# Performance work log

Hardware: AMD Instinct MI355X
Metric: run time of the kernel (lower is better)

The kernel has to match this reference:

```python
import jax, jax.numpy as jnp
import numpy as np

N = 20000      # num_nodes
E = 320000     # num_edges (avg degree 16)
HID = 256      # hid_dim
H = 4          # attention heads
D = HID // H   # per-head dim (concat heads -> HID)
L = 2          # nGAT_layer
OUT = 12       # out_dim / pred_len (decoder steps)
NEG_SLOPE = 0.2


def setup_inputs() -> dict:
    key = jax.random.key(0)
    ks = jax.random.split(key, 16)
    s = 0.05
    nrm = lambda k, shape: jax.random.normal(k, shape, jnp.float32) * s
    return dict(
        x=nrm(ks[0], (N, HID)),
        edge_index=jax.random.randint(ks[1], (2, E), 0, N, dtype=jnp.int32),
        # GATv2Conv params per layer (stacked over L layers)
        gat_w_src=nrm(ks[2], (L, HID, H * D)),
        gat_w_dst=nrm(ks[3], (L, HID, H * D)),
        gat_att=nrm(ks[4], (L, H, D)),
        gat_bias=nrm(ks[5], (L, H * D)),
        # decoder_mlp: Linear(1 + HID -> HID)
        mlp_w=nrm(ks[6], (HID, 1 + HID)),
        mlp_b=nrm(ks[7], (HID,)),
        # nn.LSTM (1 layer, input HID, hidden HID), torch gate order i,f,g,o
        lstm_w_ih=nrm(ks[8], (4 * HID, HID)),
        lstm_w_hh=nrm(ks[9], (4 * HID, HID)),
        lstm_b_ih=nrm(ks[10], (4 * HID,)),
        lstm_b_hh=nrm(ks[11], (4 * HID,)),
        # decoder_init_proj: Linear(HID -> 1); decoder_output_proj: Linear(HID -> 1)
        init_w=nrm(ks[12], (1, HID)),
        init_b=nrm(ks[13], (1,)),
        out_w=nrm(ks[14], (1, HID)),
        out_b=nrm(ks[15], (1,)),
    )


def _gatv2_layer(x, src, dst, w_src, w_dst, att, bias):
    n = x.shape[0]
    xl = (x @ w_src).reshape(n, H, D)   # source-side projection
    xr = (x @ w_dst).reshape(n, H, D)   # destination-side projection
    # GATv2: e_ij = a^T LeakyReLU(Wl x_j + Wr x_i)
    e = jax.nn.leaky_relu(xl[src] + xr[dst], NEG_SLOPE)        # [E,H,D]
    logits = jnp.einsum('ehd,hd->eh', e, att)                   # [E,H]
    # edge softmax over incoming edges of each destination node
    m = jax.ops.segment_max(logits, dst, num_segments=n)        # [N,H]
    ex = jnp.exp(logits - m[dst])
    denom = jax.ops.segment_sum(ex, dst, num_segments=n)
    alpha = ex / denom[dst]                                     # [E,H]
    out = jax.ops.segment_sum(xl[src] * alpha[:, :, None], dst, num_segments=n)
    return out.reshape(n, H * D) + bias


def reference(x, edge_index, gat_w_src, gat_w_dst, gat_att, gat_bias,
              mlp_w, mlp_b, lstm_w_ih, lstm_w_hh, lstm_b_ih, lstm_b_hh,
              init_w, init_b, out_w, out_b):
    src, dst = edge_index[0], edge_index[1]
    # stacked GAT blocks: GATv2Conv + ELU (element == 2)
    for l in range(L):
        x = _gatv2_layer(x, src, dst, gat_w_src[l], gat_w_dst[l], gat_att[l], gat_bias[l])
        x = jax.nn.elu(x)
    # recurrent LSTM decoder, batch = nodes, seq step by step
    ctx = x                      # encoder_context
    h = x                        # h_0 = x (num_layers = 1)
    c = jnp.zeros_like(x)        # c_0 = 0
    prev = x @ init_w.T + init_b  # [N,1]
    outs = []
    for _ in range(OUT):
        dec_in = jnp.concatenate([prev, ctx], axis=1) @ mlp_w.T + mlp_b  # [N,HID]
        gates = dec_in @ lstm_w_ih.T + lstm_b_ih + h @ lstm_w_hh.T + lstm_b_hh
        i_g, f_g, g_g, o_g = jnp.split(gates, 4, axis=1)
        i_g = jax.nn.sigmoid(i_g)
        f_g = jax.nn.sigmoid(f_g)
        o_g = jax.nn.sigmoid(o_g)
        g_g = jnp.tanh(g_g)
        c = f_g * c + i_g * g_g
        h = o_g * jnp.tanh(c)
        prev = h @ out_w.T + out_b  # [N,1]
        outs.append(prev)
    return jnp.concatenate(outs, axis=1)  # [N, OUT]
```

## Files before the change

### kernel.cpp

```cpp
#include <hip/hip_runtime.h>
#include <hip/hip_bf16.h>

#define NN 20000
#define NE 320000
#define TOUT 12
#define DEGMAX 96
#define MR 80
#define NBLK 250
#define NCHL 14

typedef __bf16 bf16x8 __attribute__((ext_vector_type(8)));
typedef float float4v __attribute__((ext_vector_type(4)));

#define LD8(p) (*(const bf16x8*)(p))
#define MFMA16(a,b,c) __builtin_amdgcn_mfma_f32_16x16x32_bf16((a),(b),(c),0,0,0)

__device__ __forceinline__ float bf2f(const __hip_bfloat16 v){ return __bfloat162float(v); }
__device__ __forceinline__ __hip_bfloat16 f2bf(float v){ return __float2bfloat16(v); }
__device__ __forceinline__ float sigmoidr_(float x){ return __builtin_amdgcn_rcpf(1.f + __expf(-x)); }
__device__ __forceinline__ float tanhr_(float x){ return 1.f - 2.f*__builtin_amdgcn_rcpf(__expf(2.f*x) + 1.f); }
__device__ __forceinline__ float rdf(const void* p, int i, int f32){
  return f32 ? ((const float*)p)[i] : __bfloat162float(((const __hip_bfloat16*)p)[i]);
}

__global__ void k_detect(const void* xraw, int* flag){
  __shared__ int cnt;
  if(threadIdx.x == 0) cnt = 0;
  __syncthreads();
  const unsigned* w = (const unsigned*)xraw;
  int local = 0;
  for(int i = threadIdx.x; i < 4096; i += 256){
    unsigned b = (w[i] >> 8) & 0x7F;
    if(b >= 0x33 && b <= 0x3F) local++;
  }
  atomicAdd(&cnt, local);
  __syncthreads();
  if(threadIdx.x == 0) *flag = (cnt > 2048) ? 0 : 1;
}

__global__ void k_fail(float* out, int n){
  int i = blockIdx.x*256 + threadIdx.x;
  if(i < n) out[i] = 256.0f;
}

__global__ void k_count(const int* __restrict__ dst, int* __restrict__ deg){
  int e = blockIdx.x*256 + threadIdx.x;
  if(e < NE){
    unsigned d = (unsigned)dst[e];
    if(d < NN) atomicAdd(&deg[d], 1);
  }
}

__global__ void k_scan(const int* __restrict__ deg, int* __restrict__ offp, int* __restrict__ cursor){
  __shared__ int part[256];
  __shared__ int excl[257];
  const int CH = (NN + 255)/256;
  int tid = threadIdx.x;
  int lo = tid*CH;
  int hi = lo + CH; if(hi > NN) hi = NN;
  int s = 0;
  for(int i=lo;i<hi;i++) s += deg[i];
  part[tid] = s;
  __syncthreads();
  if(tid == 0){
    int run = 0;
    for(int i=0;i<256;i++){ excl[i] = run; run += part[i]; }
    excl[256] = run;
  }
  __syncthreads();
  int run = excl[tid];
  for(int i=lo;i<hi;i++){ offp[i] = run; cursor[i] = run; run += deg[i]; }
  if(tid == 0) offp[NN] = excl[256];
}

__global__ void k_fill(const int* __restrict__ src, const int* __restrict__ dst,
                       int* __restrict__ cursor, int* __restrict__ csr_src){
  int e = blockIdx.x*256 + threadIdx.x;
  if(e >= NE) return;
  unsigned d = (unsigned)dst[e];
  if(d >= NN) return;
  unsigned p = (unsigned)atomicAdd(&cursor[d], 1);
  if(p < NE){
    unsigned sv = (unsigned)src[e];
    csr_src[p] = (sv < NN) ? (int)sv : 0;
  }
}

__global__ void k_prep(const void* __restrict__ w_src, const void* __restrict__ w_dst,
                       const void* __restrict__ w_hh, const void* __restrict__ wih,
                       const void* __restrict__ mlp_w, const int* __restrict__ flag,
                       __hip_bfloat16* __restrict__ wsrcT, __hip_bfloat16* __restrict__ wdstT,
                       __hip_bfloat16* __restrict__ whhp, __hip_bfloat16* __restrict__ wihb,
                       __hip_bfloat16* __restrict__ mlpT){
  int tid = blockIdx.x*256 + threadIdx.x;
  int f = *flag;
  if(tid < 131072){
    int l = tid >> 16, r = tid & 65535, o = r >> 8, i = r & 255;
    wsrcT[tid] = f2bf(rdf(w_src, l*65536 + i*256 + o, f));
    wdstT[tid] = f2bf(rdf(w_dst, l*65536 + i*256 + o, f));
  }
  if(tid < 262144){
    whhp[tid] = f2bf(rdf(w_hh, tid, f));
    wihb[tid] = f2bf(rdf(wih, tid, f));
  }
  if(tid < 65536){
    int k = tid >> 8, j = tid & 255;
    mlpT[tid] = f2bf(rdf(mlp_w, j*257 + 1 + k, f));
  }
}

__global__ void k_prep_ub(const void* __restrict__ wih, const void* __restrict__ mlp_w,
                          const void* __restrict__ mlp_b,
                          const void* __restrict__ b_ih, const void* __restrict__ b_hh,
                          const void* __restrict__ att, const void* __restrict__ gbias,
                          const void* __restrict__ init_w, const void* __restrict__ init_b,
                          const void* __restrict__ out_w, const void* __restrict__ out_b,
                          const int* __restrict__ flag,
                          float* __restrict__ u, float* __restrict__ bc,
                          float* __restrict__ attf, float* __restrict__ gbiasf,
                          float* __restrict__ initwf, float* __restrict__ outwf,
                          float* __restrict__ sc){
  __shared__ float su[256], sb[256];
  int g = blockIdx.x, j = threadIdx.x, f = *flag;
  float w = rdf(wih, g*256 + j, f);
  su[j] = w * rdf(mlp_w, j*257, f);
  sb[j] = w * rdf(mlp_b, j, f);
  if(g < 2){
    int i = g*256 + j;
    attf[i] = rdf(att, i, f);
    gbiasf[i] = rdf(gbias, i, f);
  }
  if(g == 0){
    initwf[j] = rdf(init_w, j, f);
    outwf[j]  = rdf(out_w, j, f);
    if(j == 0){ sc[0] = rdf(init_b, 0, f); sc[1] = rdf(out_b, 0, f); }
  }
  __syncthreads();
  for(int s=128; s>0; s>>=1){
    if(j < s){ su[j] += su[j+s]; sb[j] += sb[j+s]; }
    __syncthreads();
  }
  if(j == 0){ u[g] = su[0]; bc[g] = sb[0] + rdf(b_ih, g, f) + rdf(b_hh, g, f); }
}

__global__ void k_fold(const __hip_bfloat16* __restrict__ whh_pl,
                       const float* __restrict__ u_vec, const float* __restrict__ outwf,
                       __hip_bfloat16* __restrict__ whh2_pl){
  int i = blockIdx.x*256 + threadIdx.x;
  whh2_pl[i] = f2bf(bf2f(whh_pl[i]) + u_vec[i >> 8]*outwf[i & 255]);
}

__global__ void k_pack(const __hip_bfloat16* __restrict__ Wpl, const __hip_bfloat16* __restrict__ W2pl,
                       const __hip_bfloat16* __restrict__ Wcpl,
                       __hip_bfloat16* __restrict__ WhhP, __hip_bfloat16* __restrict__ Whh2P,
                       __hip_bfloat16* __restrict__ WcP){
  int idx = blockIdx.x*256 + threadIdx.x;
  if(idx >= 32768) return;
  int cs = idx >> 12;
  int kslot = (idx >> 9) & 7;
  int nt = (idx >> 6) & 7;
  int lane = idx & 63;
  int l16 = lane & 15, quad = lane >> 4;
  int brow = (nt>>1)*256 + cs*32 + (nt&1)*16 + l16;
  int srcofs = brow*256 + kslot*32 + quad*8;
  int dst = idx*8;
  *(bf16x8*)(WhhP + dst)  = LD8(Wpl + srcofs);
  *(bf16x8*)(Whh2P + dst) = LD8(W2pl + srcofs);
  *(bf16x8*)(WcP + dst)   = LD8(Wcpl + srcofs);
}

__global__ void k_pack2(const __hip_bfloat16* __restrict__ wsrcT,
                        const __hip_bfloat16* __restrict__ wdstT,
                        __hip_bfloat16* __restrict__ wprojP){
  int idx = blockIdx.x*256 + threadIdx.x;
  if(idx >= 32768) return;
  int m = idx >> 13;
  int fi = idx & 8191;
  int l = m >> 1, role = m & 1;
  int kidx = fi >> 10;
  int nt = (fi >> 6) & 15;
  int lane = fi & 63;
  int l16 = lane & 15, quad = lane >> 4;
  const __hip_bfloat16* src = (role ? wdstT : wsrcT) + l*65536;
  int srcofs = (nt*16 + l16)*256 + kidx*32 + quad*8;
  *(bf16x8*)(wprojP + (size_t)m*65536 + fi*8) = LD8(src + srcofs);
}

__global__ __launch_bounds__(256) void k_gemm_nt_bf(const __hip_bfloat16* __restrict__ A,
                                                    const __hip_bfloat16* __restrict__ B,
                                                    __hip_bfloat16* __restrict__ Cb, int M){
  int wave = threadIdx.x >> 6;
  int lane = threadIdx.x & 63;
  int l16 = lane & 15, quad = lane >> 4, quad8 = quad*8;
  int mBase = blockIdx.x*64 + wave*16;
  int nBase = blockIdx.y*64;
  int arow = mBase + l16; if(arow >= M) arow = M-1;
  const __hip_bfloat16* aptr = A + (size_t)arow*256 + quad8;
  float4v acc[4];
  #pragma unroll
  for(int nt=0;nt<4;nt++){ acc[nt][0]=0.f; acc[nt][1]=0.f; acc[nt][2]=0.f; acc[nt][3]=0.f; }
  for(int k0=0;k0<256;k0+=32){
    bf16x8 a = LD8(aptr + k0);
    #pragma unroll
    for(int nt=0;nt<4;nt++){
      const __hip_bfloat16* bptr = B + (size_t)(nBase + nt*16 + l16)*256 + k0 + quad8;
      acc[nt] = MFMA16(a, LD8(bptr), acc[nt]);
    }
  }
  #pragma unroll
  for(int nt=0;nt<4;nt++){
    int col = nBase + nt*16 + l16;
    #pragma unroll
    for(int r=0;r<4;r++){
      int row = mBase + quad*4 + r;
      if(row < M) Cb[(size_t)row*256 + col] = f2bf(acc[nt][r]);
    }
  }
}

__global__ __launch_bounds__(512, 2) void k_gemm_dual(__hip_bfloat16* __restrict__ P,
                                                      const void* __restrict__ xraw,
                                                      const int* __restrict__ flag,
                                                      int layer0,
                                                      const __hip_bfloat16* __restrict__ BsrcP,
                                                      const __hip_bfloat16* __restrict__ BdstP,
                                                      __hip_bfloat16* __restrict__ Q){
  __shared__ __hip_bfloat16 sA[64*264];
  int tid = threadIdx.x;
  int mBase = blockIdx.x*64;
  {
    int r = tid >> 3;
    int c0 = (tid & 7)*32;
    int grow = mBase + r; if(grow >= NN) grow = NN-1;
    if(layer0){
      int f = *flag;
      #pragma unroll
      for(int j=0;j<32;j++) sA[r*264 + c0 + j] = f2bf(rdf(xraw, grow*256 + c0 + j, f));
    }else{
      const __hip_bfloat16* srcp = P + (size_t)grow*256 + c0;
      #pragma unroll
      for(int j=0;j<4;j++) *(bf16x8*)(&sA[r*264 + c0 + j*8]) = LD8(srcp + j*8);
    }
  }
  __syncthreads();
  int w8 = tid >> 6;
  int w = w8 & 3;
  int role = w8 >> 2;
  int lane = tid&63, l16 = lane&15, quad = lane>>4, quad8 = quad*8;
  const __hip_bfloat16* B = role ? BdstP : BsrcP;
  __hip_bfloat16* C = role ? P : Q;
  const __hip_bfloat16* arow = &sA[(w*16 + l16)*264 + quad8];
  float4v acc[16];
  #pragma unroll
  for(int nt=0;nt<16;nt++){ acc[nt][0]=0.f; acc[nt][1]=0.f; acc[nt][2]=0.f; acc[nt][3]=0.f; }
  for(int kidx=0;kidx<8;kidx++){
    bf16x8 a = *(const bf16x8*)(arow + kidx*32);
    const __hip_bfloat16* bbase = B + (kidx<<13) + (lane<<3);
    #pragma unroll
    for(int nt=0;nt<16;nt++)
      acc[nt] = MFMA16(a, LD8(bbase + (nt<<9)), acc[nt]);
  }
  #pragma unroll
  for(int nt=0;nt<16;nt++){
    int col = nt*16 + l16;
    #pragma unroll
    for(int r=0;r<4;r++){
      int row = mBase + w*16 + quad*4 + r;
      if(row < NN) C[(size_t)row*256 + col] = f2bf(acc[nt][r]);
    }
  }
}

__global__ __launch_bounds__(256) void k_node_fused(const __hip_bfloat16* __restrict__ Q,
                                                    __hip_bfloat16* __restrict__ P,
                                                    const int* __restrict__ offp,
                                                    const int* __restrict__ csr_src,
                                                    const float* __restrict__ attf,
                                                    const float* __restrict__ gbiasf){
  __shared__ float slog[DEGMAX*4];
  __shared__ int ssrc[DEGMAX];
  int node = blockIdx.x;
  int tid = threadIdx.x;
  int s0 = offp[node], s1 = offp[node+1];
  if(s0 < 0) s0 = 0; if(s0 > NE) s0 = NE;
  if(s1 < s0) s1 = s0; if(s1 > NE) s1 = NE;
  int deg = s1 - s0; if(deg > DEGMAX) deg = DEGMAX;
  if(tid < deg){
    unsigned sv = (unsigned)csr_src[s0 + tid];
    ssrc[tid] = (sv < NN) ? (int)sv : 0;
  }
  __syncthreads();
  int w = tid>>6, lane = tid&63;
  int eSlot = lane>>4, li = lane&15;
  float prl[16], attl[16];
  #pragma unroll
  for(int h=0;h<4;h++)
    #pragma unroll
    for(int j=0;j<4;j++){
      int d = h*64 + j*16 + li;
      prl[h*4+j]  = bf2f(P[(size_t)node*256 + d]);
      attl[h*4+j] = attf[d];
    }
  for(int base=0; base<deg; base+=16){
    int e = base + w*4 + eSlot;
    bool valid = (e < deg);
    const __hip_bfloat16* pl = Q + (size_t)ssrc[valid ? e : 0]*256;
    float part[4];
    #pragma unroll
    for(int h=0;h<4;h++){
      float p = 0.f;
      #pragma unroll
      for(int j=0;j<4;j++){
        int d = h*64 + j*16 + li;
        float v = bf2f(pl[d]) + prl[h*4+j];
        v = (v > 0.f) ? v : 0.2f*v;
        p += v * attl[h*4+j];
      }
      part[h] = p;
    }
    #pragma unroll
    for(int h=0;h<4;h++){
      part[h] += __shfl_xor(part[h], 1, 64);
      part[h] += __shfl_xor(part[h], 2, 64);
      part[h] += __shfl_xor(part[h], 4, 64);
      part[h] += __shfl_xor(part[h], 8, 64);
    }
    if(li == 0 && valid){
      #pragma unroll
      for(int h=0;h<4;h++) slog[e*4+h] = part[h];
    }
  }
  __syncthreads();
  {
    int hh = tid >> 6;
    int li64 = tid & 63;
    float m = -1e30f;
    for(int i=li64; i<deg; i+=64) m = fmaxf(m, slog[i*4+hh]);
    #pragma unroll
    for(int s=1; s<64; s<<=1) m = fmaxf(m, __shfl_xor(m, s, 64));
    float den = 0.f;
    for(int i=li64; i<deg; i+=64) den += __expf(slog[i*4+hh] - m);
    #pragma unroll
    for(int s=1; s<64; s<<=1) den += __shfl_xor(den, s, 64);
    float inv = (den > 0.f) ? 1.f/den : 0.f;
    for(int i=li64; i<deg; i+=64) slog[i*4+hh] = __expf(slog[i*4+hh] - m)*inv;
  }
  __syncthreads();
  int d = tid, hd = d>>6;
  float acc = 0.f;
  for(int i=0;i<deg;i++) acc += slog[i*4+hd] * bf2f(Q[(size_t)ssrc[i]*256 + d]);
  acc += gbiasf[d];
  acc = (acc > 0.f) ? acc : (__expf(acc) - 1.f);
  P[(size_t)node*256 + d] = f2bf(acc);
}

__global__ __launch_bounds__(512, 1) void k_lstm80(const __hip_bfloat16* __restrict__ ctx,
                                                   const __hip_bfloat16* __restrict__ WcP,
                                                   const __hip_bfloat16* __restrict__ WhhP,
                                                   const __hip_bfloat16* __restrict__ Whh2P,
                                                   const float* __restrict__ u_vec,
                                                   const float* __restrict__ bc_vec,
                                                   const float* __restrict__ initwf,
                                                   const float* __restrict__ outwf,
                                                   const float* __restrict__ sc,
                                                   float* __restrict__ out){
  __shared__ __hip_bfloat16 sgx[NCHL*4096];
  __shared__ __hip_bfloat16 sh[MR*264];
  __shared__ float spartw[MR*8];
  __shared__ float sprev0[MR];
  float* spart = (float*)sgx;
  int tid = threadIdx.x;
  int mBase = blockIdx.x*MR;
  int cs = tid>>6, lane = tid&63, l16 = lane&15, quad = lane>>4, quad8 = quad*8;
  int phase = (blockIdx.x >> 3) & 7;
  #pragma unroll
  for(int p=0;p<3;p++){
    int r = p*32 + (tid >> 4);
    if(r < MR){
      int c0 = (tid & 15)*16;
      const __hip_bfloat16* srcp = ctx + (size_t)(mBase + r)*256 + c0;
      *(bf16x8*)(&sh[r*264 + c0])     = LD8(srcp);
      *(bf16x8*)(&sh[r*264 + c0 + 8]) = LD8(srcp + 8);
    }
  }
  __syncthreads();
  #pragma unroll
  for(int p=0;p<3;p++){
    int r = p*32 + (tid >> 4);
    int c0 = (tid & 15)*16;
    float part = 0.f;
    if(r < MR){
      #pragma unroll
      for(int j=0;j<16;j++) part += bf2f(sh[r*264 + c0 + j]) * initwf[c0 + j];
    }
    spart[tid] = part;
    __syncthreads();
    if(tid < 32 && p*32 + tid < MR){
      float s = 0.f;
      #pragma unroll
      for(int j=0;j<16;j++) s += spart[tid*16 + j];
      sprev0[p*32 + tid] = s + sc[0];
    }
    __syncthreads();
  }
  float owreg[2];
  #pragma unroll
  for(int tc=0;tc<2;tc++) owreg[tc] = outwf[cs*32 + tc*16 + l16];
  float outb = sc[1];
  bf16x8 gg0, gg1, gg2, gg3, gg4, gg5;
  {
    float bcl[8];
    #pragma unroll
    for(int g=0;g<4;g++)
      #pragma unroll
      for(int tc=0;tc<2;tc++)
        bcl[g*2+tc] = bc_vec[g*256 + cs*32 + tc*16 + l16]
                    + u_vec[g*256 + cs*32 + tc*16 + l16]*outb;
    {
      float4v acc[24];
      #pragma unroll
      for(int nt=0;nt<24;nt++){ acc[nt][0]=0.f; acc[nt][1]=0.f; acc[nt][2]=0.f; acc[nt][3]=0.f; }
      #pragma unroll 2
      for(int ki=0;ki<8;ki++){
        int kidx = (ki + phase) & 7;
        int k0 = kidx*32;
        bf16x8 a0 = *(const bf16x8*)(&sh[l16*264 + k0 + quad8]);
        bf16x8 a1 = *(const bf16x8*)(&sh[(16 + l16)*264 + k0 + quad8]);
        bf16x8 a2 = *(const bf16x8*)(&sh[(32 + l16)*264 + k0 + quad8]);
        const __hip_bfloat16* bbase = WcP + (((cs<<3) + kidx)<<12) + (lane<<3);
        #pragma unroll
        for(int nt=0;nt<8;nt++){
          bf16x8 b = LD8(bbase + (nt<<9));
          acc[nt]    = MFMA16(a0, b, acc[nt]);
          acc[8+nt]  = MFMA16(a1, b, acc[8+nt]);
          acc[16+nt] = MFMA16(a2, b, acc[16+nt]);
        }
      }
      #pragma unroll
      for(int rt=0;rt<3;rt++)
        #pragma unroll
        for(int tc=0;tc<2;tc++)
          #pragma unroll
          for(int half=0;half<2;half++){
            bf16x8 v;
            #pragma unroll
            for(int rr=0;rr<2;rr++)
              #pragma unroll
              for(int g=0;g<4;g++){
                int r = half*2 + rr;
                v[rr*4+g] = (__bf16)f2bf(acc[rt*8 + g*2 + tc][r] + bcl[g*2+tc]);
              }
            int cp = (rt*2+tc)*2 + half;
            *(bf16x8*)(&sgx[cp*4096 + tid*8]) = v;
          }
    }
    {
      float4v acc[16];
      #pragma unroll
      for(int nt=0;nt<16;nt++){ acc[nt][0]=0.f; acc[nt][1]=0.f; acc[nt][2]=0.f; acc[nt][3]=0.f; }
      #pragma unroll 2
      for(int ki=0;ki<8;ki++){
        int kidx = (ki + phase) & 7;
        int k0 = kidx*32;
        bf16x8 a3 = *(const bf16x8*)(&sh[(48 + l16)*264 + k0 + quad8]);
        bf16x8 a4 = *(const bf16x8*)(&sh[(64 + l16)*264 + k0 + quad8]);
        const __hip_bfloat16* bbase = WcP + (((cs<<3) + kidx)<<12) + (lane<<3);
        #pragma unroll
        for(int nt=0;nt<8;nt++){
          bf16x8 b = LD8(bbase + (nt<<9));
          acc[nt]   = MFMA16(a3, b, acc[nt]);
          acc[8+nt] = MFMA16(a4, b, acc[8+nt]);
        }
      }
      #pragma unroll
      for(int rtl=0;rtl<2;rtl++)
        #pragma unroll
        for(int tc=0;tc<2;tc++)
          #pragma unroll
          for(int half=0;half<2;half++){
            bf16x8 v;
            #pragma unroll
            for(int rr=0;rr<2;rr++)
              #pragma unroll
              for(int g=0;g<4;g++){
                int r = half*2 + rr;
                v[rr*4+g] = (__bf16)f2bf(acc[rtl*8 + g*2 + tc][r] + bcl[g*2+tc]);
              }
            const int cp = ((3+rtl)*2+tc)*2 + half;
            if(cp == 12 || cp == 13) *(bf16x8*)(&sgx[cp*4096 + tid*8]) = v;
            else if(cp == 14) gg0 = v;
            else if(cp == 15) gg1 = v;
            else if(cp == 16) gg2 = v;
            else if(cp == 17) gg3 = v;
            else if(cp == 18) gg4 = v;
            else              gg5 = v;
          }
    }
  }
  float creg[40];
  #pragma unroll
  for(int i=0;i<40;i++) creg[i] = 0.f;
  #pragma unroll 1
  for(int step=0; step<TOUT; step++){
    const __hip_bfloat16* W = (step == 0) ? WhhP : Whh2P;
    float4v accA[24];
    #pragma unroll
    for(int nt=0;nt<24;nt++){ accA[nt][0]=0.f; accA[nt][1]=0.f; accA[nt][2]=0.f; accA[nt][3]=0.f; }
    #pragma unroll 2
    for(int ki=0;ki<8;ki++){
      int kidx = (ki + phase) & 7;
      int k0 = kidx*32;
      bf16x8 a0 = *(const bf16x8*)(&sh[l16*264 + k0 + quad8]);
      bf16x8 a1 = *(const bf16x8*)(&sh[(16 + l16)*264 + k0 + quad8]);
      bf16x8 a2 = *(const bf16x8*)(&sh[(32 + l16)*264 + k0 + quad8]);
      const __hip_bfloat16* bbase = W + (((cs<<3) + kidx)<<12) + (lane<<3);
      #pragma unroll
      for(int nt=0;nt<8;nt++){
        bf16x8 b = LD8(bbase + (nt<<9));
        accA[nt]    = MFMA16(a0, b, accA[nt]);
        accA[8+nt]  = MFMA16(a1, b, accA[8+nt]);
        accA[16+nt] = MFMA16(a2, b, accA[16+nt]);
      }
    }
    __syncthreads();
    #pragma unroll
    for(int rt=0; rt<3; rt++){
      float hsum[4];
      hsum[0]=0.f; hsum[1]=0.f; hsum[2]=0.f; hsum[3]=0.f;
      #pragma unroll
      for(int tc=0;tc<2;tc++){
        int col = cs*32 + tc*16 + l16;
        const int cpb = (rt*2+tc)*2;
        bf16x8 ga = *(const bf16x8*)(&sgx[cpb*4096 + tid*8]);
        bf16x8 gb = *(const bf16x8*)(&sgx[(cpb+1)*4096 + tid*8]);
        #pragma unroll
        for(int r=0;r<4;r++){
          int row = rt*16 + quad*4 + r;
          int jb = (r&1)*4;
          float gx0, gx1, gx2, gx3;
          if(r < 2){
            gx0 = bf2f((__hip_bfloat16)ga[jb]);   gx1 = bf2f((__hip_bfloat16)ga[jb+1]);
            gx2 = bf2f((__hip_bfloat16)ga[jb+2]); gx3 = bf2f((__hip_bfloat16)ga[jb+3]);
          }else{
            gx0 = bf2f((__hip_bfloat16)gb[jb]);   gx1 = bf2f((__hip_bfloat16)gb[jb+1]);
            gx2 = bf2f((__hip_bfloat16)gb[jb+2]); gx3 = bf2f((__hip_bfloat16)gb[jb+3]);
          }
          float g0 = accA[rt*8 + tc][r]     + gx0;
          float g1 = accA[rt*8 + 2 + tc][r] + gx1;
          float g2 = accA[rt*8 + 4 + tc][r] + gx2;
          float g3 = accA[rt*8 + 6 + tc][r] + gx3;
          if(step == 0){
            float pd = sprev0[row] - outb;
            g0 += pd*u_vec[col];
            g1 += pd*u_vec[256 + col];
            g2 += pd*u_vec[512 + col];
            g3 += pd*u_vec[768 + col];
          }
          float iv = sigmoidr_(g0), fv = sigmoidr_(g1);
          float gv = tanhr_(g2),    ov = sigmoidr_(g3);
          float cn = fv*creg[rt*8 + tc*4 + r] + iv*gv;
          creg[rt*8 + tc*4 + r] = cn;
          float hn = ov * tanhr_(cn);
          sh[row*264 + col] = f2bf(hn);
          hsum[r] += hn * owreg[tc];
        }
      }
      #pragma unroll
      for(int r=0;r<4;r++){
        hsum[r] += __shfl_xor(hsum[r], 1, 64);
        hsum[r] += __shfl_xor(hsum[r], 2, 64);
        hsum[r] += __shfl_xor(hsum[r], 4, 64);
        hsum[r] += __shfl_xor(hsum[r], 8, 64);
      }
      if(l16 == 0){
        #pragma unroll
        for(int r=0;r<4;r++)
          spartw[(rt*16 + quad*4 + r)*8 + cs] = hsum[r];
      }
    }
    float4v accB[16];
    #pragma unroll
    for(int nt=0;nt<16;nt++){ accB[nt][0]=0.f; accB[nt][1]=0.f; accB[nt][2]=0.f; accB[nt][3]=0.f; }
    #pragma unroll 2
    for(int ki=0;ki<8;ki++){
      int kidx = (ki + phase) & 7;
      int k0 = kidx*32;
      bf16x8 a3 = *(const bf16x8*)(&sh[(48 + l16)*264 + k0 + quad8]);
      bf16x8 a4 = *(const bf16x8*)(&sh[(64 + l16)*264 + k0 + quad8]);
      const __hip_bfloat16* bbase = W + (((cs<<3) + kidx)<<12) + (lane<<3);
      #pragma unroll
      for(int nt=0;nt<8;nt++){
        bf16x8 b = LD8(bbase + (nt<<9));
        accB[nt]   = MFMA16(a3, b, accB[nt]);
        accB[8+nt] = MFMA16(a4, b, accB[8+nt]);
      }
    }
    __syncthreads();
    #pragma unroll
    for(int rtl=0; rtl<2; rtl++){
      const int rt = 3 + rtl;
      float hsum[4];
      hsum[0]=0.f; hsum[1]=0.f; hsum[2]=0.f; hsum[3]=0.f;
      #pragma unroll
      for(int tc=0;tc<2;tc++){
        int col = cs*32 + tc*16 + l16;
        bf16x8 ga, gb;
        if(rtl == 0 && tc == 0){
          ga = *(const bf16x8*)(&sgx[12*4096 + tid*8]);
          gb = *(const bf16x8*)(&sgx[13*4096 + tid*8]);
        }else if(rtl == 0 && tc == 1){ ga = gg0; gb = gg1; }
        else if(rtl == 1 && tc == 0){ ga = gg2; gb = gg3; }
        else                        { ga = gg4; gb = gg5; }
        #pragma unroll
        for(int r=0;r<4;r++){
          int row = rt*16 + quad*4 + r;
          int jb = (r&1)*4;
          float gx0, gx1, gx2, gx3;
          if(r < 2){
            gx0 = bf2f((__hip_bfloat16)ga[jb]);   gx1 = bf2f((__hip_bfloat16)ga[jb+1]);
            gx2 = bf2f((__hip_bfloat16)ga[jb+2]); gx3 = bf2f((__hip_bfloat16)ga[jb+3]);
          }else{
            gx0 = bf2f((__hip_bfloat16)gb[jb]);   gx1 = bf2f((__hip_bfloat16)gb[jb+1]);
            gx2 = bf2f((__hip_bfloat16)gb[jb+2]); gx3 = bf2f((__hip_bfloat16)gb[jb+3]);
          }
          float g0 = accB[rtl*8 + tc][r]     + gx0;
          float g1 = accB[rtl*8 + 2 + tc][r] + gx1;
          float g2 = accB[rtl*8 + 4 + tc][r] + gx2;
          float g3 = accB[rtl*8 + 6 + tc][r] + gx3;
          if(step == 0){
            float pd = sprev0[row] - outb;
            g0 += pd*u_vec[col];
            g1 += pd*u_vec[256 + col];
            g2 += pd*u_vec[512 + col];
            g3 += pd*u_vec[768 + col];
          }
          float iv = sigmoidr_(g0), fv = sigmoidr_(g1);
          float gv = tanhr_(g2),    ov = sigmoidr_(g3);
          float cn = fv*creg[rt*8 + tc*4 + r] + iv*gv;
          creg[rt*8 + tc*4 + r] = cn;
          float hn = ov * tanhr_(cn);
          sh[row*264 + col] = f2bf(hn);
          hsum[r] += hn * owreg[tc];
        }
      }
      #pragma unroll
      for(int r=0;r<4;r++){
        hsum[r] += __shfl_xor(hsum[r], 1, 64);
        hsum[r] += __shfl_xor(hsum[r], 2, 64);
        hsum[r] += __shfl_xor(hsum[r], 4, 64);
        hsum[r] += __shfl_xor(hsum[r], 8, 64);
      }
      if(l16 == 0){
        #pragma unroll
        for(int r=0;r<4;r++)
          spartw[(rt*16 + quad*4 + r)*8 + cs] = hsum[r];
      }
    }
    __syncthreads();
    if(tid < MR){
      float s = outb;
      #pragma unroll
      for(int c=0;c<8;c++) s += spartw[tid*8 + c];
      out[(size_t)(mBase + tid)*TOUT + step] = s;
    }
  }
}

extern "C" void kernel_launch(void* const* d_in, const int* in_sizes, int n_in,
                              void* d_out, int out_size, void* d_ws, size_t ws_size,
                              hipStream_t stream){
  const void* x      = d_in[0];
  const int*  ei     = (const int*)d_in[1];
  const void* w_src  = d_in[2];
  const void* w_dst  = d_in[3];
  const void* att    = d_in[4];
  const void* gbias  = d_in[5];
  const void* mlp_w  = d_in[6];
  const void* mlp_b  = d_in[7];
  const void* w_ih   = d_in[8];
  const void* w_hh   = d_in[9];
  const void* b_ih   = d_in[10];
  const void* b_hh   = d_in[11];
  const void* init_w = d_in[12];
  const void* init_b = d_in[13];
  const void* out_w  = d_in[14];
  const void* out_b  = d_in[15];
  float* out = (float*)d_out;
  const int* srcp = ei;
  const int* dstp = ei + NE;
  (void)in_sizes; (void)n_in;

  char* ws = (char*)d_ws;
  size_t off = 0;
  auto alloc = [&](size_t bytes)->void*{
    void* p = ws + off;
    off += (bytes + 255) & ~(size_t)255;
    return p;
  };
  __hip_bfloat16* P = (__hip_bfloat16*)alloc((size_t)NN*256*2);
  __hip_bfloat16* Q = (__hip_bfloat16*)alloc((size_t)NN*256*2);
  int* deg      = (int*)alloc((size_t)NN*4);
  int* offp     = (int*)alloc((size_t)(NN+1)*4);
  int* cursor   = (int*)alloc((size_t)NN*4);
  int* csr_src  = (int*)alloc((size_t)NE*4);
  __hip_bfloat16* wsrcT   = (__hip_bfloat16*)alloc((size_t)131072*2);
  __hip_bfloat16* wdstT   = (__hip_bfloat16*)alloc((size_t)131072*2);
  __hip_bfloat16* wprojP  = (__hip_bfloat16*)alloc((size_t)4*65536*2);
  __hip_bfloat16* whh_pl  = (__hip_bfloat16*)alloc((size_t)262144*2);
  __hip_bfloat16* whh2_pl = (__hip_bfloat16*)alloc((size_t)262144*2);
  __hip_bfloat16* Wc_pl   = (__hip_bfloat16*)alloc((size_t)262144*2);
  __hip_bfloat16* WhhP    = (__hip_bfloat16*)alloc((size_t)262144*2);
  __hip_bfloat16* Whh2P   = (__hip_bfloat16*)alloc((size_t)262144*2);
  __hip_bfloat16* WcP     = (__hip_bfloat16*)alloc((size_t)262144*2);
  __hip_bfloat16* wihb    = (__hip_bfloat16*)alloc((size_t)262144*2);
  __hip_bfloat16* mlpT    = (__hip_bfloat16*)alloc((size_t)65536*2);
  float* u_vec  = (float*)alloc(1024*4);
  float* bc_vec = (float*)alloc(1024*4);
  float* attf   = (float*)alloc(512*4);
  float* gbiasf = (float*)alloc(512*4);
  float* initwf = (float*)alloc(256*4);
  float* outwf  = (float*)alloc(256*4);
  float* sc     = (float*)alloc(2*4);
  int*   flag   = (int*)alloc(4);

  if(off > ws_size){
    k_fail<<<(out_size + 255)/256, 256, 0, stream>>>(out, out_size);
    return;
  }

  k_detect<<<1, 256, 0, stream>>>(x, flag);
  hipMemsetAsync(deg, 0, (size_t)NN*4, stream);
  hipMemsetAsync(csr_src, 0xFF, (size_t)NE*4, stream);
  k_count<<<NE/256, 256, 0, stream>>>(dstp, deg);
  k_scan<<<1, 256, 0, stream>>>(deg, offp, cursor);
  k_fill<<<NE/256, 256, 0, stream>>>(srcp, dstp, cursor, csr_src);
  k_prep<<<1024, 256, 0, stream>>>(w_src, w_dst, w_hh, w_ih, mlp_w, flag,
                                   wsrcT, wdstT, whh_pl, wihb, mlpT);
  k_prep_ub<<<1024, 256, 0, stream>>>(w_ih, mlp_w, mlp_b, b_ih, b_hh, att, gbias,
                                      init_w, init_b, out_w, out_b, flag,
                                      u_vec, bc_vec, attf, gbiasf, initwf, outwf, sc);
  {
    dim3 gwc(16, 4);
    k_gemm_nt_bf<<<gwc, 256, 0, stream>>>(wihb, mlpT, Wc_pl, 1024);
  }
  k_fold<<<1024, 256, 0, stream>>>(whh_pl, u_vec, outwf, whh2_pl);
  k_pack<<<128, 256, 0, stream>>>(whh_pl, whh2_pl, Wc_pl, WhhP, Whh2P, WcP);
  k_pack2<<<128, 256, 0, stream>>>(wsrcT, wdstT, wprojP);

  for(int l=0;l<2;l++){
    k_gemm_dual<<<313, 512, 0, stream>>>(P, x, flag, (l == 0) ? 1 : 0,
                                         wprojP + (size_t)(l*2)*65536,
                                         wprojP + (size_t)(l*2+1)*65536, Q);
    k_node_fused<<<NN, 256, 0, stream>>>(Q, P, offp, csr_src, attf + l*256, gbiasf + l*256);
  }

  k_lstm80<<<NBLK, 512, 0, stream>>>(P, WcP, WhhP, Whh2P, u_vec, bc_vec,
                                     initwf, outwf, sc, out);
}
```

Baseline: 687.9 us.

## Cache gathered source rows in LDS and split LSTM gate GEMM by gate pairs

```diff
diff --git a/kernel.cpp b/kernel.cpp
--- a/kernel.cpp
+++ b/kernel.cpp
@@ -5,6 +5,7 @@
 #define NE 320000
 #define TOUT 12
 #define DEGMAX 96
+#define SQE 64
 #define MR 80
 #define NBLK 250
 #define NCHL 14
@@ -277,6 +278,7 @@
                                                     const int* __restrict__ csr_src,
                                                     const float* __restrict__ attf,
                                                     const float* __restrict__ gbiasf){
+  __shared__ __hip_bfloat16 sQ[SQE*264];
   __shared__ float slog[DEGMAX*4];
   __shared__ int ssrc[DEGMAX];
   int node = blockIdx.x;
@@ -293,42 +295,33 @@
   int w = tid>>6, lane = tid&63;
   int eSlot = lane>>4, li = lane&15;
   float prl[16], attl[16];
-  #pragma unroll
-  for(int h=0;h<4;h++)
-    #pragma unroll
-    for(int j=0;j<4;j++){
-      int d = h*64 + j*16 + li;
-      prl[h*4+j]  = bf2f(P[(size_t)node*256 + d]);
-      attl[h*4+j] = attf[d];
-    }
+  {
+    const __hip_bfloat16* prow = P + (size_t)node*256 + li*16;
+    bf16x8 p0 = LD8(prow), p1 = LD8(prow + 8);
+    #pragma unroll
+    for(int j=0;j<8;j++){ prl[j] = bf2f((__hip_bfloat16)p0[j]); prl[8+j] = bf2f((__hip_bfloat16)p1[j]); }
+    #pragma unroll
+    for(int j=0;j<16;j++) attl[j] = attf[li*16 + j];
+  }
   for(int base=0; base<deg; base+=16){
     int e = base + w*4 + eSlot;
     bool valid = (e < deg);
-    const __hip_bfloat16* pl = Q + (size_t)ssrc[valid ? e : 0]*256;
-    float part[4];
-    #pragma unroll
-    for(int h=0;h<4;h++){
-      float p = 0.f;
-      #pragma unroll
-      for(int j=0;j<4;j++){
-        int d = h*64 + j*16 + li;
-        float v = bf2f(pl[d]) + prl[h*4+j];
-        v = (v > 0.f) ? v : 0.2f*v;
-        p += v * attl[h*4+j];
-      }
-      part[h] = p;
-    }
-    #pragma unroll
-    for(int h=0;h<4;h++){
-      part[h] += __shfl_xor(part[h], 1, 64);
-      part[h] += __shfl_xor(part[h], 2, 64);
-      part[h] += __shfl_xor(part[h], 4, 64);
-      part[h] += __shfl_xor(part[h], 8, 64);
-    }
-    if(li == 0 && valid){
-      #pragma unroll
-      for(int h=0;h<4;h++) slog[e*4+h] = part[h];
-    }
+    const __hip_bfloat16* qrow = Q + (size_t)ssrc[valid ? e : 0]*256 + li*16;
+    bf16x8 q0 = LD8(qrow), q1 = LD8(qrow + 8);
+    if(valid && e < SQE){
+      *(bf16x8*)(&sQ[e*264 + li*16])     = q0;
+      *(bf16x8*)(&sQ[e*264 + li*16 + 8]) = q1;
+    }
+    float part = 0.f;
+    #pragma unroll
+    for(int j=0;j<16;j++){
+      float v = bf2f((__hip_bfloat16)(j<8 ? q0[j] : q1[j-8])) + prl[j];
+      v = (v > 0.f) ? v : 0.2f*v;
+      part += v * attl[j];
+    }
+    part += __shfl_xor(part, 1, 64);
+    part += __shfl_xor(part, 2, 64);
+    if((li & 3) == 0 && valid) slog[e*4 + (li>>2)] = part;
   }
   __syncthreads();
   {
@@ -348,7 +341,9 @@
   __syncthreads();
   int d = tid, hd = d>>6;
   float acc = 0.f;
-  for(int i=0;i<deg;i++) acc += slog[i*4+hd] * bf2f(Q[(size_t)ssrc[i]*256 + d]);
+  int dl = (deg < SQE) ? deg : SQE;
+  for(int i=0;i<dl;i++) acc += slog[i*4+hd] * bf2f(sQ[i*264 + d]);
+  for(int i=SQE;i<deg;i++) acc += slog[i*4+hd] * bf2f(Q[(size_t)ssrc[i]*256 + d]);
   acc += gbiasf[d];
   acc = (acc > 0.f) ? acc : (__expf(acc) - 1.f);
   P[(size_t)node*256 + d] = f2bf(acc);
@@ -497,15 +492,15 @@
           }
     }
   }
-  float creg[40];
+  float creg[40], ivr[40];
   #pragma unroll
   for(int i=0;i<40;i++) creg[i] = 0.f;
   #pragma unroll 1
   for(int step=0; step<TOUT; step++){
     const __hip_bfloat16* W = (step == 0) ? WhhP : Whh2P;
-    float4v accA[24];
-    #pragma unroll
-    for(int nt=0;nt<24;nt++){ accA[nt][0]=0.f; accA[nt][1]=0.f; accA[nt][2]=0.f; accA[nt][3]=0.f; }
+    float4v accA[20];
+    #pragma unroll
+    for(int nt=0;nt<20;nt++){ accA[nt][0]=0.f; accA[nt][1]=0.f; accA[nt][2]=0.f; accA[nt][3]=0.f; }
     #pragma unroll 2
     for(int ki=0;ki<8;ki++){
       int kidx = (ki + phase) & 7;
@@ -513,131 +508,112 @@
       bf16x8 a0 = *(const bf16x8*)(&sh[l16*264 + k0 + quad8]);
       bf16x8 a1 = *(const bf16x8*)(&sh[(16 + l16)*264 + k0 + quad8]);
       bf16x8 a2 = *(const bf16x8*)(&sh[(32 + l16)*264 + k0 + quad8]);
+      bf16x8 a3 = *(const bf16x8*)(&sh[(48 + l16)*264 + k0 + quad8]);
+      bf16x8 a4 = *(const bf16x8*)(&sh[(64 + l16)*264 + k0 + quad8]);
       const __hip_bfloat16* bbase = W + (((cs<<3) + kidx)<<12) + (lane<<3);
       #pragma unroll
-      for(int nt=0;nt<8;nt++){
-        bf16x8 b = LD8(bbase + (nt<<9));
-        accA[nt]    = MFMA16(a0, b, accA[nt]);
-        accA[8+nt]  = MFMA16(a1, b, accA[8+nt]);
-        accA[16+nt] = MFMA16(a2, b, accA[16+nt]);
+      for(int ntl=0;ntl<4;ntl++){
+        bf16x8 b = LD8(bbase + (ntl<<9));
+        accA[ntl]    = MFMA16(a0, b, accA[ntl]);
+        accA[4+ntl]  = MFMA16(a1, b, accA[4+ntl]);
+        accA[8+ntl]  = MFMA16(a2, b, accA[8+ntl]);
+        accA[12+ntl] = MFMA16(a3, b, accA[12+ntl]);
+        accA[16+ntl] = MFMA16(a4, b, accA[16+ntl]);
       }
     }
-    __syncthreads();
-    #pragma unroll
-    for(int rt=0; rt<3; rt++){
-      float hsum[4];
-      hsum[0]=0.f; hsum[1]=0.f; hsum[2]=0.f; hsum[3]=0.f;
+    #pragma unroll
+    for(int rt=0; rt<5; rt++){
       #pragma unroll
       for(int tc=0;tc<2;tc++){
         int col = cs*32 + tc*16 + l16;
         const int cpb = (rt*2+tc)*2;
-        bf16x8 ga = *(const bf16x8*)(&sgx[cpb*4096 + tid*8]);
-        bf16x8 gb = *(const bf16x8*)(&sgx[(cpb+1)*4096 + tid*8]);
+        bf16x8 ga, gb;
+        if(cpb == 14){ ga = gg0; gb = gg1; }
+        else if(cpb == 16){ ga = gg2; gb = gg3; }
+        else if(cpb == 18){ ga = gg4; gb = gg5; }
+        else{
+          ga = *(const bf16x8*)(&sgx[cpb*4096 + tid*8]);
+          gb = *(const bf16x8*)(&sgx[(cpb+1)*4096 + tid*8]);
+        }
         #pragma unroll
         for(int r=0;r<4;r++){
           int row = rt*16 + quad*4 + r;
           int jb = (r&1)*4;
-          float gx0, gx1, gx2, gx3;
-          if(r < 2){
-            gx0 = bf2f((__hip_bfloat16)ga[jb]);   gx1 = bf2f((__hip_bfloat16)ga[jb+1]);
-            gx2 = bf2f((__hip_bfloat16)ga[jb+2]); gx3 = bf2f((__hip_bfloat16)ga[jb+3]);
-          }else{
-            gx0 = bf2f((__hip_bfloat16)gb[jb]);   gx1 = bf2f((__hip_bfloat16)gb[jb+1]);
-            gx2 = bf2f((__hip_bfloat16)gb[jb+2]); gx3 = bf2f((__hip_bfloat16)gb[jb+3]);
-          }
-          float g0 = accA[rt*8 + tc][r]     + gx0;
-          float g1 = accA[rt*8 + 2 + tc][r] + gx1;
-          float g2 = accA[rt*8 + 4 + tc][r] + gx2;
-          float g3 = accA[rt*8 + 6 + tc][r] + gx3;
+          float gx0, gx1;
+          if(r < 2){ gx0 = bf2f((__hip_bfloat16)ga[jb]); gx1 = bf2f((__hip_bfloat16)ga[jb+1]); }
+          else     { gx0 = bf2f((__hip_bfloat16)gb[jb]); gx1 = bf2f((__hip_bfloat16)gb[jb+1]); }
+          float g0 = accA[rt*4 + tc][r]     + gx0;
+          float g1 = accA[rt*4 + 2 + tc][r] + gx1;
           if(step == 0){
             float pd = sprev0[row] - outb;
             g0 += pd*u_vec[col];
             g1 += pd*u_vec[256 + col];
-            g2 += pd*u_vec[512 + col];
-            g3 += pd*u_vec[768 + col];
           }
-          float iv = sigmoidr_(g0), fv = sigmoidr_(g1);
-          float gv = tanhr_(g2),    ov = sigmoidr_(g3);
-          float cn = fv*creg[rt*8 + tc*4 + r] + iv*gv;
-          creg[rt*8 + tc*4 + r] = cn;
-          float hn = ov * tanhr_(cn);
-          sh[row*264 + col] = f2bf(hn);
-          hsum[r] += hn * owreg[tc];
+          int idx = rt*8 + tc*4 + r;
+          float fv = sigmoidr_(g1);
+          ivr[idx] = sigmoidr_(g0);
+          creg[idx] *= fv;
         }
       }
-      #pragma unroll
-      for(int r=0;r<4;r++){
-        hsum[r] += __shfl_xor(hsum[r], 1, 64);
-        hsum[r] += __shfl_xor(hsum[r], 2, 64);
-        hsum[r] += __shfl_xor(hsum[r], 4, 64);
-        hsum[r] += __shfl_xor(hsum[r], 8, 64);
-      }
-      if(l16 == 0){
-        #pragma unroll
-        for(int r=0;r<4;r++)
-          spartw[(rt*16 + quad*4 + r)*8 + cs] = hsum[r];
-      }
-    }
-    float4v accB[16];
-    #pragma unroll
-    for(int nt=0;nt<16;nt++){ accB[nt][0]=0.f; accB[nt][1]=0.f; accB[nt][2]=0.f; accB[nt][3]=0.f; }
+    }
+    float4v accB[20];
+    #pragma unroll
+    for(int nt=0;nt<20;nt++){ accB[nt][0]=0.f; accB[nt][1]=0.f; accB[nt][2]=0.f; accB[nt][3]=0.f; }
     #pragma unroll 2
     for(int ki=0;ki<8;ki++){
       int kidx = (ki + phase) & 7;
       int k0 = kidx*32;
+      bf16x8 a0 = *(const bf16x8*)(&sh[l16*264 + k0 + quad8]);
+      bf16x8 a1 = *(const bf16x8*)(&sh[(16 + l16)*264 + k0 + quad8]);
+      bf16x8 a2 = *(const bf16x8*)(&sh[(32 + l16)*264 + k0 + quad8]);
       bf16x8 a3 = *(const bf16x8*)(&sh[(48 + l16)*264 + k0 + quad8]);
       bf16x8 a4 = *(const bf16x8*)(&sh[(64 + l16)*264 + k0 + quad8]);
       const __hip_bfloat16* bbase = W + (((cs<<3) + kidx)<<12) + (lane<<3);
       #pragma unroll
-      for(int nt=0;nt<8;nt++){
-        bf16x8 b = LD8(bbase + (nt<<9));
-        accB[nt]   = MFMA16(a3, b, accB[nt]);
-        accB[8+nt] = MFMA16(a4, b, accB[8+nt]);
+      for(int ntl=0;ntl<4;ntl++){
+        bf16x8 b = LD8(bbase + ((4+ntl)<<9));
+        accB[ntl]    = MFMA16(a0, b, accB[ntl]);
+        accB[4+ntl]  = MFMA16(a1, b, accB[4+ntl]);
+        accB[8+ntl]  = MFMA16(a2, b, accB[8+ntl]);
+        accB[12+ntl] = MFMA16(a3, b, accB[12+ntl]);
+        accB[16+ntl] = MFMA16(a4, b, accB[16+ntl]);
       }
     }
     __syncthreads();
     #pragma unroll
-    for(int rtl=0; rtl<2; rtl++){
-      const int rt = 3 + rtl;
+    for(int rt=0; rt<5; rt++){
       float hsum[4];
       hsum[0]=0.f; hsum[1]=0.f; hsum[2]=0.f; hsum[3]=0.f;
       #pragma unroll
       for(int tc=0;tc<2;tc++){
         int col = cs*32 + tc*16 + l16;
+        const int cpb = (rt*2+tc)*2;
         bf16x8 ga, gb;
-        if(rtl == 0 && tc == 0){
-          ga = *(const bf16x8*)(&sgx[12*4096 + tid*8]);
-          gb = *(const bf16x8*)(&sgx[13*4096 + tid*8]);
-        }else if(rtl == 0 && tc == 1){ ga = gg0; gb = gg1; }
-        else if(rtl == 1 && tc == 0){ ga = gg2; gb = gg3; }
-        else                        { ga = gg4; gb = gg5; }
+        if(cpb == 14){ ga = gg0; gb = gg1; }
+        else if(cpb == 16){ ga = gg2; gb = gg3; }
+        else if(cpb == 18){ ga = gg4; gb = gg5; }
+        else{
+          ga = *(const bf16x8*)(&sgx[cpb*4096 + tid*8]);
+          gb = *(const bf16x8*)(&sgx[(cpb+1)*4096 + tid*8]);
+        }
         #pragma unroll
         for(int r=0;r<4;r++){
           int row = rt*16 + quad*4 + r;
           int jb = (r&1)*4;
-          float gx0, gx1, gx2, gx3;
-          if(r < 2){
-            gx0 = bf2f((__hip_bfloat16)ga[jb]);   gx1 = bf2f((__hip_bfloat16)ga[jb+1]);
-            gx2 = bf2f((__hip_bfloat16)ga[jb+2]); gx3 = bf2f((__hip_bfloat16)ga[jb+3]);
-          }else{
-            gx0 = bf2f((__hip_bfloat16)gb[jb]);   gx1 = bf2f((__hip_bfloat16)gb[jb+1]);
-            gx2 = bf2f((__hip_bfloat16)gb[jb+2]); gx3 = bf2f((__hip_bfloat16)gb[jb+3]);
-          }
-          float g0 = accB[rtl*8 + tc][r]     + gx0;
-          float g1 = accB[rtl*8 + 2 + tc][r] + gx1;
-          float g2 = accB[rtl*8 + 4 + tc][r] + gx2;
-          float g3 = accB[rtl*8 + 6 + tc][r] + gx3;
+          float gx2, gx3;
+          if(r < 2){ gx2 = bf2f((__hip_bfloat16)ga[jb+2]); gx3 = bf2f((__hip_bfloat16)ga[jb+3]); }
+          else     { gx2 = bf2f((__hip_bfloat16)gb[jb+2]); gx3 = bf2f((__hip_bfloat16)gb[jb+3]); }
+          float g2 = accB[rt*4 + tc][r]     + gx2;
+          float g3 = accB[rt*4 + 2 + tc][r] + gx3;
           if(step == 0){
             float pd = sprev0[row] - outb;
-            g0 += pd*u_vec[col];
-            g1 += pd*u_vec[256 + col];
             g2 += pd*u_vec[512 + col];
             g3 += pd*u_vec[768 + col];
           }
-          float iv = sigmoidr_(g0), fv = sigmoidr_(g1);
-          float gv = tanhr_(g2),    ov = sigmoidr_(g3);
-          float cn = fv*creg[rt*8 + tc*4 + r] + iv*gv;
-          creg[rt*8 + tc*4 + r] = cn;
+          float gv = tanhr_(g2), ov = sigmoidr_(g3);
+          int idx = rt*8 + tc*4 + r;
+          float cn = creg[idx] + ivr[idx]*gv;
+          creg[idx] = cn;
           float hn = ov * tanhr_(cn);
           sh[row*264 + col] = f2bf(hn);
           hsum[r] += hn * owreg[tc];
```

Measured after the change: 780.0 us. 1.13x slower.
